# Kernel optimization log

Hardware: AMD Instinct MI355X
Metric: run time of the kernel (lower is better)

The kernel has to match this reference:

```python
import jax, jax.numpy as jnp
import numpy as np

VOCAB = 32000
D_MODEL = 1024


def setup_inputs() -> dict:
    key = jax.random.key(0)
    k = jax.random.split(key, 8)
    B, H, T, S = 8, 16, 128, 512
    src = jax.random.randint(k[0], (B, S), 0, VOCAB)
    decode_output = jax.random.normal(k[1], (B, T, D_MODEL), dtype=jnp.float32)
    decode_attn = jax.random.uniform(k[2], (B, H, T, S), dtype=jnp.float32)
    memory = jax.random.normal(k[3], (B, S, D_MODEL), dtype=jnp.float32)
    W_gen = jax.random.normal(k[4], (VOCAB, D_MODEL), dtype=jnp.float32) * (1.0 / np.sqrt(D_MODEL))
    b_gen = jnp.zeros((VOCAB,), dtype=jnp.float32)
    W_prob = jax.random.normal(k[5], (1, 2 * D_MODEL), dtype=jnp.float32) * (1.0 / np.sqrt(2 * D_MODEL))
    b_prob = jnp.zeros((1,), dtype=jnp.float32)
    return {"src": src, "decode_output": decode_output, "decode_attn": decode_attn,
            "memory": memory, "W_gen": W_gen, "b_gen": b_gen,
            "W_prob": W_prob, "b_prob": b_prob}


def reference(src, decode_output, decode_attn, memory, W_gen, b_gen, W_prob, b_prob):
    # mean over heads: [B, T, S]
    attn = jnp.mean(decode_attn, axis=1)
    B, T, S = attn.shape
    V = W_gen.shape[0]

    # generation logits: [B, T, V]
    gen_logits = jnp.einsum('btd,vd->btv', decode_output, W_gen) + b_gen

    # context vector: [B, T, D]
    context = jnp.einsum('bts,bsd->btd', attn, memory)

    # scatter-add copy distribution over vocab: [B, T, V]
    src_exp = jnp.broadcast_to(src[:, None, :], (B, T, S))  # token ids per step
    b_idx = jnp.arange(B)[:, None, None]
    t_idx = jnp.arange(T)[None, :, None]
    copy_logits = jnp.zeros((B, T, V), dtype=attn.dtype).at[b_idx, t_idx, src_exp].add(attn)

    # copy gate: sigmoid(Linear([context; decode_output])) -> [B, T, 1]
    cat = jnp.concatenate([context, decode_output], axis=-1)
    prob = jax.nn.sigmoid(jnp.einsum('btd,od->bto', cat, W_prob) + b_prob)

    gen_p = prob * jax.nn.softmax(gen_logits, axis=-1)
    copy_p = (1.0 - prob) * jax.nn.softmax(copy_logits, axis=-1)
    final = gen_p + copy_p
    return jnp.log(final).reshape(-1, V)
```

## Files before the change

### kernel.cpp

```cpp
#include <hip/hip_runtime.h>
#include <hip/hip_bf16.h>
#include <cstddef>
#include <cstdint>

#define BB 8
#define HH 16
#define TT 128
#define SS 512
#define DD 1024
#define VV 32000
#define MM (BB * TT)

typedef float f32x4 __attribute__((ext_vector_type(4)));
typedef short short8v __attribute__((ext_vector_type(8)));
typedef unsigned short ushort8v __attribute__((ext_vector_type(8)));

__device__ __forceinline__ unsigned short f2bf(float x) {
    __hip_bfloat16 h = __float2bfloat16(x);
    return __builtin_bit_cast(unsigned short, h);
}
__device__ __forceinline__ float bf2f(unsigned short u) {
    unsigned int x = ((unsigned int)u) << 16;
    return __builtin_bit_cast(float, x);
}

__device__ __forceinline__ float wave_sum(float v) {
#pragma unroll
    for (int o = 1; o < 64; o <<= 1) v += __shfl_xor(v, o);
    return v;
}
__device__ __forceinline__ float wave_max(float v) {
#pragma unroll
    for (int o = 1; o < 64; o <<= 1) v = fmaxf(v, __shfl_xor(v, o));
    return v;
}
__device__ __forceinline__ float block_sum(float v, float* red, int tid) {
    v = wave_sum(v);
    __syncthreads();
    if ((tid & 63) == 0) red[tid >> 6] = v;
    __syncthreads();
    return red[0] + red[1] + red[2] + red[3];
}
__device__ __forceinline__ float block_max(float v, float* red, int tid) {
    v = wave_max(v);
    __syncthreads();
    if ((tid & 63) == 0) red[tid >> 6] = v;
    __syncthreads();
    return fmaxf(fmaxf(red[0], red[1]), fmaxf(red[2], red[3]));
}

__global__ void k_pm_init(int* pos_map, float* zg) {
    int i = blockIdx.x * 256 + threadIdx.x;
    if (i < BB * VV) pos_map[i] = 0x7fffffff;
    if (i < MM) zg[i] = 0.0f;
}

__global__ void k_pm_build(const int* __restrict__ src, int* pos_map) {
    int b = blockIdx.x, s = threadIdx.x;
    int tok = src[b * SS + s];
    atomicMin(&pos_map[b * VV + tok], s);
}

__global__ __launch_bounds__(256) void k_cast(const float* __restrict__ in,
                                              unsigned short* __restrict__ outp, int n8) {
    int stride = gridDim.x * 256;
    for (int i = blockIdx.x * 256 + threadIdx.x; i < n8; i += stride) {
        const float4* p = reinterpret_cast<const float4*>(in + (size_t)i * 8);
        float4 a = p[0], b = p[1];
        ushort8v u;
        u[0] = f2bf(a.x); u[1] = f2bf(a.y); u[2] = f2bf(a.z); u[3] = f2bf(a.w);
        u[4] = f2bf(b.x); u[5] = f2bf(b.y); u[6] = f2bf(b.z); u[7] = f2bf(b.w);
        *reinterpret_cast<ushort8v*>(outp + (size_t)i * 8) = u;
    }
}

__global__ __launch_bounds__(256) void k_vecdots(const float* __restrict__ memory,
                                                 const float* __restrict__ dec,
                                                 const float* __restrict__ wprob,
                                                 float* mw, float* dw) {
    int row = blockIdx.x * 4 + (threadIdx.x >> 6);
    int lane = threadIdx.x & 63;
    const float4* srcv;
    const float4* wv;
    if (row < BB * SS) {
        srcv = reinterpret_cast<const float4*>(memory + (size_t)row * DD);
        wv = reinterpret_cast<const float4*>(wprob);
    } else {
        srcv = reinterpret_cast<const float4*>(dec + (size_t)(row - BB * SS) * DD);
        wv = reinterpret_cast<const float4*>(wprob + DD);
    }
    float sum = 0.f;
#pragma unroll
    for (int k = 0; k < 4; ++k) {
        int idx = lane + 64 * k;
        float4 a = srcv[idx];
        float4 w = wv[idx];
        sum += a.x * w.x + a.y * w.y + a.z * w.z + a.w * w.w;
    }
    sum = wave_sum(sum);
    if (lane == 0) {
        if (row < BB * SS) mw[row] = sum;
        else dw[row - BB * SS] = sum;
    }
}

__global__ __launch_bounds__(256) void k_row(const float* __restrict__ dattn,
                                             const int* __restrict__ src,
                                             const int* __restrict__ pos_map,
                                             const float* __restrict__ mw,
                                             const float* __restrict__ dw,
                                             const float* __restrict__ bprob,
                                             float* __restrict__ e_vals,
                                             float* __restrict__ prob,
                                             float* __restrict__ zc,
                                             float* __restrict__ c0) {
    int bt = blockIdx.x;
    int b = bt >> 7;
    int t = bt & 127;
    int tid = threadIdx.x;
    __shared__ float a_row[SS];
    __shared__ float vals[SS];
    __shared__ float red[4];

    for (int s = tid; s < SS; s += 256) {
        const float* base = dattn + ((size_t)b * HH * TT + t) * SS + s;
        float sum = 0.f;
#pragma unroll
        for (int h = 0; h < HH; ++h) sum += base[(size_t)h * TT * SS];
        a_row[s] = sum * 0.0625f;
        vals[s] = 0.f;
    }
    __syncthreads();
    for (int s = tid; s < SS; s += 256) {
        int rep = pos_map[b * VV + src[b * SS + s]];
        atomicAdd(&vals[rep], a_row[s]);
    }
    __syncthreads();
    float psum = 0.f;
    for (int s = tid; s < SS; s += 256) psum += a_row[s] * mw[b * SS + s];
    psum = block_sum(psum, red, tid);
    float z = psum + dw[bt] + bprob[0];
    float p = 1.0f / (1.0f + __expf(-z));
    float mxv = -3.4e38f;
    for (int s = tid; s < SS; s += 256) {
        int rep = pos_map[b * VV + src[b * SS + s]];
        if (rep == s) mxv = fmaxf(mxv, vals[s]);
    }
    mxv = block_max(mxv, red, tid);
    float m_c = fmaxf(0.0f, mxv);
    float sexp = 0.f, cnt = 0.f;
    for (int s = tid; s < SS; s += 256) {
        int rep = pos_map[b * VV + src[b * SS + s]];
        float e = 0.0f;
        if (rep == s) {
            e = __expf(vals[s] - m_c);
            sexp += e;
            cnt += 1.0f;
        }
        e_vals[(size_t)bt * SS + s] = e;
    }
    sexp = block_sum(sexp, red, tid);
    cnt = block_sum(cnt, red, tid);
    if (tid == 0) {
        prob[bt] = p;
        zc[bt] = ((float)VV - cnt) * __expf(-m_c) + sexp;
        c0[bt] = __expf(-m_c);
    }
}

#define NKT 32
#define BUFE 12288

#define AS1 __attribute__((address_space(1)))
#define AS3 __attribute__((address_space(3)))

template <int EPI>
__global__ __launch_bounds__(512, 4) void k_gemm_bf(const unsigned short* __restrict__ Abf,
                                                    const unsigned short* __restrict__ Wbf,
                                                    const float* __restrict__ bgen,
                                                    float* __restrict__ out,
                                                    unsigned short* __restrict__ ebuf,
                                                    float* __restrict__ zg) {
    __shared__ unsigned short lds[3 * BUFE];

    int tid = threadIdx.x;
    int p = blockIdx.x;
    int wgid = (p & 7) * 125 + (p >> 3);
    int mt = wgid & 7, nt = wgid >> 3;
    int m0 = mt * 128, v0 = nt * 256;

    int lane = tid & 63, w = tid >> 6;
    int wm = w & 1, wn = w >> 1;

    int srow = tid >> 2;
    int schunk = (tid & 3) ^ ((tid >> 3) & 3);
    const unsigned short* gA = Abf + (size_t)(m0 + srow) * DD + schunk * 8;
    const unsigned short* gB = Wbf + (size_t)(v0 + srow) * DD + schunk * 8;

#define STAGE(T, BI) do {                                                              \
    size_t ko_ = (size_t)(T) * 32;                                                     \
    __builtin_amdgcn_global_load_lds(                                                  \
        (const AS1 void*)(gA + ko_),                                                   \
        (AS3 void*)(lds + (BI) * BUFE + tid * 8), 16, 0, 0);                           \
    __builtin_amdgcn_global_load_lds(                                                  \
        (const AS1 void*)(gB + ko_),                                                   \
        (AS3 void*)(lds + (BI) * BUFE + 4096 + tid * 8), 16, 0, 0);                    \
    __builtin_amdgcn_global_load_lds(                                                  \
        (const AS1 void*)(gB + (size_t)128 * DD + ko_),                                \
        (AS3 void*)(lds + (BI) * BUFE + 8192 + tid * 8), 16, 0, 0);                    \
} while (0)

    int lr = lane & 15, kg = lane >> 4;
    int xr = (lr >> 1) & 3;
    const unsigned short* arow = lds + (wm * 64 + lr) * 32 + ((kg ^ xr) << 3);
    const unsigned short* brow = lds + 4096 + (wn * 64 + lr) * 32 + ((kg ^ xr) << 3);

    f32x4 acc[4][4] = {};

#define ITER(T, BI, DO_STAGE, VM)  do {                                                \
    __builtin_amdgcn_s_barrier();                                                      \
    short8v af[4], bfr[4];                                                             \
    _Pragma("unroll")                                                                  \
    for (int i = 0; i < 4; ++i)                                                        \
        af[i] = *reinterpret_cast<const short8v*>(arow + (BI) * BUFE + i * 512);       \
    _Pragma("unroll")                                                                  \
    for (int j = 0; j < 4; ++j)                                                        \
        bfr[j] = *reinterpret_cast<const short8v*>(brow + (BI) * BUFE + j * 512);      \
    if (DO_STAGE) STAGE((T) + 2, ((BI) + 2) % 3);                                      \
    asm volatile("s_waitcnt lgkmcnt(0)" ::: "memory");                                 \
    __builtin_amdgcn_sched_barrier(0);                                                 \
    __builtin_amdgcn_s_setprio(1);                                                     \
    _Pragma("unroll")                                                                  \
    for (int i = 0; i < 4; ++i)                                                        \
        _Pragma("unroll")                                                              \
        for (int j = 0; j < 4; ++j)                                                    \
            acc[i][j] = __builtin_amdgcn_mfma_f32_16x16x32_bf16(af[i], bfr[j], acc[i][j], 0, 0, 0); \
    __builtin_amdgcn_s_setprio(0);                                                     \
    if ((VM) == 3) asm volatile("s_waitcnt vmcnt(3)" ::: "memory");                    \
    else if ((VM) == 0) asm volatile("s_waitcnt vmcnt(0)" ::: "memory");               \
} while (0)

    STAGE(0, 0);
    STAGE(1, 1);
    asm volatile("s_waitcnt vmcnt(3)" ::: "memory");

    for (int t = 0; t < NKT - 2; t += 3) {
        ITER(t + 0, 0, true, 3);
        ITER(t + 1, 1, true, 3);
        ITER(t + 2, 2, true, 3);
    }
    ITER(30, 0, false, 0);
    ITER(31, 1, false, -1);
#undef ITER
#undef STAGE

    int colb = lane & 15, rgrp = lane >> 4;
#pragma unroll
    for (int i = 0; i < 4; ++i) {
        float es0 = 0.f, es1 = 0.f, es2 = 0.f, es3 = 0.f;
        int gmb = m0 + wm * 64 + i * 16 + rgrp * 4;
#pragma unroll
        for (int j = 0; j < 4; ++j) {
            int gv = v0 + wn * 64 + j * 16 + colb;
            float bgj = bgen[gv];
            float v0f = acc[i][j][0] + bgj;
            float v1f = acc[i][j][1] + bgj;
            float v2f = acc[i][j][2] + bgj;
            float v3f = acc[i][j][3] + bgj;
            float e0 = __expf(v0f), e1 = __expf(v1f), e2 = __expf(v2f), e3 = __expf(v3f);
            if constexpr (EPI == 1) {
                ebuf[(size_t)(gmb + 0) * VV + gv] = f2bf(e0);
                ebuf[(size_t)(gmb + 1) * VV + gv] = f2bf(e1);
                ebuf[(size_t)(gmb + 2) * VV + gv] = f2bf(e2);
                ebuf[(size_t)(gmb + 3) * VV + gv] = f2bf(e3);
            } else {
                out[(size_t)(gmb + 0) * VV + gv] = v0f;
                out[(size_t)(gmb + 1) * VV + gv] = v1f;
                out[(size_t)(gmb + 2) * VV + gv] = v2f;
                out[(size_t)(gmb + 3) * VV + gv] = v3f;
            }
            es0 += e0; es1 += e1; es2 += e2; es3 += e3;
        }
        float es[4] = {es0, es1, es2, es3};
#pragma unroll
        for (int rr = 0; rr < 4; ++rr) {
            float e = es[rr];
            e += __shfl_xor(e, 1); e += __shfl_xor(e, 2);
            e += __shfl_xor(e, 4); e += __shfl_xor(e, 8);
            if (colb == 0) atomicAdd(&zg[gmb + rr], e);
        }
    }
}

#define FBb 128
#define FLDK 40

__global__ __launch_bounds__(256) void k_gemm_f32(const float* __restrict__ A,
                                                  const float* __restrict__ Wg,
                                                  const float* __restrict__ bgen,
                                                  float* __restrict__ out,
                                                  float* __restrict__ zg) {
    __shared__ unsigned short As[FBb * FLDK];
    __shared__ unsigned short Bs[FBb * FLDK];
    int tid = threadIdx.x;
    int bid = blockIdx.x;
    int mt = bid & 7;
    int nt = bid >> 3;
    int m0 = mt * FBb, v0 = nt * FBb;
    int lane = tid & 63, wid = tid >> 6;
    int wr = (wid >> 1) * 64, wc = (wid & 1) * 64;
    int lr = lane & 15, lk = (lane >> 4) << 3;
    int r = tid >> 1, c0 = (tid & 1) << 4;

    f32x4 acc[4][4] = {};

    for (int k0 = 0; k0 < DD; k0 += 32) {
        {
            const float4* pa = reinterpret_cast<const float4*>(A + (size_t)(m0 + r) * DD + k0 + c0);
            float4 x0 = pa[0], x1 = pa[1], x2 = pa[2], x3 = pa[3];
            ushort8v u0, u1;
            u0[0] = f2bf(x0.x); u0[1] = f2bf(x0.y); u0[2] = f2bf(x0.z); u0[3] = f2bf(x0.w);
            u0[4] = f2bf(x1.x); u0[5] = f2bf(x1.y); u0[6] = f2bf(x1.z); u0[7] = f2bf(x1.w);
            u1[0] = f2bf(x2.x); u1[1] = f2bf(x2.y); u1[2] = f2bf(x2.z); u1[3] = f2bf(x2.w);
            u1[4] = f2bf(x3.x); u1[5] = f2bf(x3.y); u1[6] = f2bf(x3.z); u1[7] = f2bf(x3.w);
            *reinterpret_cast<ushort8v*>(&As[r * FLDK + c0]) = u0;
            *reinterpret_cast<ushort8v*>(&As[r * FLDK + c0 + 8]) = u1;

            const float4* pb = reinterpret_cast<const float4*>(Wg + (size_t)(v0 + r) * DD + k0 + c0);
            float4 y0 = pb[0], y1 = pb[1], y2 = pb[2], y3 = pb[3];
            ushort8v w0, w1;
            w0[0] = f2bf(y0.x); w0[1] = f2bf(y0.y); w0[2] = f2bf(y0.z); w0[3] = f2bf(y0.w);
            w0[4] = f2bf(y1.x); w0[5] = f2bf(y1.y); w0[6] = f2bf(y1.z); w0[7] = f2bf(y1.w);
            w1[0] = f2bf(y2.x); w1[1] = f2bf(y2.y); w1[2] = f2bf(y2.z); w1[3] = f2bf(y2.w);
            w1[4] = f2bf(y3.x); w1[5] = f2bf(y3.y); w1[6] = f2bf(y3.z); w1[7] = f2bf(y3.w);
            *reinterpret_cast<ushort8v*>(&Bs[r * FLDK + c0]) = w0;
            *reinterpret_cast<ushort8v*>(&Bs[r * FLDK + c0 + 8]) = w1;
        }
        __syncthreads();

        short8v af[4], bfr[4];
#pragma unroll
        for (int i = 0; i < 4; ++i)
            af[i] = *reinterpret_cast<const short8v*>(&As[(wr + i * 16 + lr) * FLDK + lk]);
#pragma unroll
        for (int j = 0; j < 4; ++j)
            bfr[j] = *reinterpret_cast<const short8v*>(&Bs[(wc + j * 16 + lr) * FLDK + lk]);
#pragma unroll
        for (int i = 0; i < 4; ++i)
#pragma unroll
            for (int j = 0; j < 4; ++j)
                acc[i][j] = __builtin_amdgcn_mfma_f32_16x16x32_bf16(af[i], bfr[j], acc[i][j], 0, 0, 0);
        __syncthreads();
    }

    int colb = lane & 15;
    int rgrp = lane >> 4;
#pragma unroll
    for (int i = 0; i < 4; ++i) {
        float es0 = 0.f, es1 = 0.f, es2 = 0.f, es3 = 0.f;
        int gmb = m0 + wr + i * 16 + rgrp * 4;
#pragma unroll
        for (int j = 0; j < 4; ++j) {
            int gv = v0 + wc + j * 16 + colb;
            float bgj = bgen[gv];
            float v0f = acc[i][j][0] + bgj;
            float v1f = acc[i][j][1] + bgj;
            float v2f = acc[i][j][2] + bgj;
            float v3f = acc[i][j][3] + bgj;
            out[(size_t)(gmb + 0) * VV + gv] = v0f;
            out[(size_t)(gmb + 1) * VV + gv] = v1f;
            out[(size_t)(gmb + 2) * VV + gv] = v2f;
            out[(size_t)(gmb + 3) * VV + gv] = v3f;
            es0 += __expf(v0f); es1 += __expf(v1f);
            es2 += __expf(v2f); es3 += __expf(v3f);
        }
        float es[4] = {es0, es1, es2, es3};
#pragma unroll
        for (int rr = 0; rr < 4; ++rr) {
            float e = es[rr];
            e += __shfl_xor(e, 1); e += __shfl_xor(e, 2);
            e += __shfl_xor(e, 4); e += __shfl_xor(e, 8);
            if (colb == 0) atomicAdd(&zg[gmb + rr], e);
        }
    }
}

template <int RD16>
__global__ __launch_bounds__(256) void k_final(float* __restrict__ gen,
                                               const unsigned short* __restrict__ ebuf,
                                               const int* __restrict__ pos_map,
                                               const float* __restrict__ e_vals,
                                               const float* __restrict__ prob,
                                               const float* __restrict__ zc,
                                               const float* __restrict__ c0,
                                               const float* __restrict__ zg) {
    int m = blockIdx.x;
    int b = m >> 7;
    int tid = threadIdx.x;
    float p = prob[m];
    float A1 = p / zg[m];
    float A2 = (1.0f - p) / zc[m];
    float cc = c0[m];
    const float* ev = e_vals + (size_t)m * SS;
    float4* row = reinterpret_cast<float4*>(gen + (size_t)m * VV);
    const int4* pm = reinterpret_cast<const int4*>(pos_map + b * VV);
    if constexpr (RD16 == 1) {
        const ushort8v* erow = reinterpret_cast<const ushort8v*>(ebuf + (size_t)m * VV);
        for (int i = tid; i < VV / 8; i += 256) {
            ushort8v ee = erow[i];
            int4 rp0 = pm[2 * i], rp1 = pm[2 * i + 1];
            float4 o0, o1;
            o0.x = __logf(A1 * bf2f(ee[0]) + A2 * ((rp0.x < SS) ? ev[rp0.x] : cc));
            o0.y = __logf(A1 * bf2f(ee[1]) + A2 * ((rp0.y < SS) ? ev[rp0.y] : cc));
            o0.z = __logf(A1 * bf2f(ee[2]) + A2 * ((rp0.z < SS) ? ev[rp0.z] : cc));
            o0.w = __logf(A1 * bf2f(ee[3]) + A2 * ((rp0.w < SS) ? ev[rp0.w] : cc));
            o1.x = __logf(A1 * bf2f(ee[4]) + A2 * ((rp1.x < SS) ? ev[rp1.x] : cc));
            o1.y = __logf(A1 * bf2f(ee[5]) + A2 * ((rp1.y < SS) ? ev[rp1.y] : cc));
            o1.z = __logf(A1 * bf2f(ee[6]) + A2 * ((rp1.z < SS) ? ev[rp1.z] : cc));
            o1.w = __logf(A1 * bf2f(ee[7]) + A2 * ((rp1.w < SS) ? ev[rp1.w] : cc));
            row[2 * i] = o0;
            row[2 * i + 1] = o1;
        }
    } else {
        for (int i = tid; i < VV / 4; i += 256) {
            float4 g = row[i];
            int4 rp = pm[i];
            float4 o;
            o.x = __logf(A1 * __expf(g.x) + A2 * ((rp.x < SS) ? ev[rp.x] : cc));
            o.y = __logf(A1 * __expf(g.y) + A2 * ((rp.y < SS) ? ev[rp.y] : cc));
            o.z = __logf(A1 * __expf(g.z) + A2 * ((rp.z < SS) ? ev[rp.z] : cc));
            o.w = __logf(A1 * __expf(g.w) + A2 * ((rp.w < SS) ? ev[rp.w] : cc));
            row[i] = o;
        }
    }
}

extern "C" void kernel_launch(void* const* d_in, const int* in_sizes, int n_in,
                              void* d_out, int out_size, void* d_ws, size_t ws_size,
                              hipStream_t stream) {
    const int* src = (const int*)d_in[0];
    const float* dec = (const float*)d_in[1];
    const float* dattn = (const float*)d_in[2];
    const float* mem = (const float*)d_in[3];
    const float* wgen = (const float*)d_in[4];
    const float* bgen = (const float*)d_in[5];
    const float* wprob = (const float*)d_in[6];
    const float* bprob = (const float*)d_in[7];
    float* out = (float*)d_out;
    char* ws = (char*)d_ws;

    int* pos_map = (int*)(ws + 0);
    float* e_vals = (float*)(ws + 1048576);
    float* mw   = (float*)(ws + 3145728);
    float* dw   = (float*)(ws + 3145728 + 16384);
    float* prob = (float*)(ws + 3145728 + 20480);
    float* zc   = (float*)(ws + 3145728 + 24576);
    float* c0   = (float*)(ws + 3145728 + 28672);
    float* zg   = (float*)(ws + 3145728 + 32768);
    unsigned short* Wbf = (unsigned short*)(ws + 3211264);
    unsigned short* Abf = (unsigned short*)(ws + 3211264 + 65536000);
    unsigned short* Ebf = (unsigned short*)(ws + 3211264 + 65536000 + 2097152);
    const size_t NEEDED  = 3211264ull + 65536000ull + 2097152ull;
    const size_t NEEDED2 = NEEDED + 65536000ull;

    k_pm_init<<<(BB * VV + 255) / 256, 256, 0, stream>>>(pos_map, zg);
    k_pm_build<<<BB, SS, 0, stream>>>(src, pos_map);
    k_vecdots<<<(BB * SS + MM) / 4, 256, 0, stream>>>(mem, dec, wprob, mw, dw);
    k_row<<<MM, 256, 0, stream>>>(dattn, src, pos_map, mw, dw, bprob, e_vals, prob, zc, c0);

    if (ws_size >= NEEDED) {
        k_cast<<<2048, 256, 0, stream>>>(wgen, Wbf, VV * DD / 8);
        k_cast<<<512, 256, 0, stream>>>(dec, Abf, MM * DD / 8);
        if (ws_size >= NEEDED2) {
            k_gemm_bf<1><<<(MM / 128) * (VV / 256), 512, 0, stream>>>(Abf, Wbf, bgen, out, Ebf, zg);
            k_final<1><<<MM, 256, 0, stream>>>(out, Ebf, pos_map, e_vals, prob, zc, c0, zg);
        } else {
            k_gemm_bf<0><<<(MM / 128) * (VV / 256), 512, 0, stream>>>(Abf, Wbf, bgen, out, Ebf, zg);
            k_final<0><<<MM, 256, 0, stream>>>(out, Ebf, pos_map, e_vals, prob, zc, c0, zg);
        }
    } else {
        k_gemm_f32<<<(MM / FBb) * (VV / FBb), 256, 0, stream>>>(dec, wgen, bgen, out, zg);
        k_final<0><<<MM, 256, 0, stream>>>(out, Ebf, pos_map, e_vals, prob, zc, c0, zg);
    }
}
```

Baseline: 224.0 us.

## Merge setup kernels into one launch, vectorize head-mean loads, relax MFMA wait

Fuses position-map build, gate vector dots, and both bf16 casts into a single block-partitioned setup kernel, replacing four small launches with one. The head-mean loop in the row kernel now reads float2 per thread. In the GEMM inner step, A/B fragment loads are interleaved and the explicit lgkmcnt wait and sched_barrier are dropped so the compiler can overlap LDS reads with MFMAs. Removing the explicit wait relies on the compiler inserting the right waits; the fused kernel also runs the W cast on fewer, larger blocks.

```diff
diff --git a/kernel.cpp b/kernel.cpp
--- a/kernel.cpp
+++ b/kernel.cpp
@@ -55,52 +55,67 @@
     if (i < MM) zg[i] = 0.0f;
 }
 
-__global__ void k_pm_build(const int* __restrict__ src, int* pos_map) {
-    int b = blockIdx.x, s = threadIdx.x;
-    int tok = src[b * SS + s];
-    atomicMin(&pos_map[b * VV + tok], s);
-}
-
-__global__ __launch_bounds__(256) void k_cast(const float* __restrict__ in,
-                                              unsigned short* __restrict__ outp, int n8) {
-    int stride = gridDim.x * 256;
-    for (int i = blockIdx.x * 256 + threadIdx.x; i < n8; i += stride) {
-        const float4* p = reinterpret_cast<const float4*>(in + (size_t)i * 8);
-        float4 a = p[0], b = p[1];
-        ushort8v u;
-        u[0] = f2bf(a.x); u[1] = f2bf(a.y); u[2] = f2bf(a.z); u[3] = f2bf(a.w);
-        u[4] = f2bf(b.x); u[5] = f2bf(b.y); u[6] = f2bf(b.z); u[7] = f2bf(b.w);
-        *reinterpret_cast<ushort8v*>(outp + (size_t)i * 8) = u;
-    }
-}
-
-__global__ __launch_bounds__(256) void k_vecdots(const float* __restrict__ memory,
-                                                 const float* __restrict__ dec,
-                                                 const float* __restrict__ wprob,
-                                                 float* mw, float* dw) {
-    int row = blockIdx.x * 4 + (threadIdx.x >> 6);
-    int lane = threadIdx.x & 63;
-    const float4* srcv;
-    const float4* wv;
-    if (row < BB * SS) {
-        srcv = reinterpret_cast<const float4*>(memory + (size_t)row * DD);
-        wv = reinterpret_cast<const float4*>(wprob);
+__global__ __launch_bounds__(512) void k_setup(const int* __restrict__ src,
+                                               int* __restrict__ pos_map,
+                                               const float* __restrict__ memory,
+                                               const float* __restrict__ dec,
+                                               const float* __restrict__ wprob,
+                                               float* __restrict__ mw,
+                                               float* __restrict__ dw,
+                                               const float* __restrict__ wgen,
+                                               unsigned short* __restrict__ Wbf,
+                                               unsigned short* __restrict__ Abf) {
+    int blk = blockIdx.x, tid = threadIdx.x;
+    if (blk < 8) {
+        int tok = src[blk * SS + tid];
+        atomicMin(&pos_map[blk * VV + tok], tid);
+    } else if (blk < 648) {
+        int row = (blk - 8) * 8 + (tid >> 6);
+        int lane = tid & 63;
+        const float4* srcv;
+        const float4* wv;
+        if (row < BB * SS) {
+            srcv = reinterpret_cast<const float4*>(memory + (size_t)row * DD);
+            wv = reinterpret_cast<const float4*>(wprob);
+        } else {
+            srcv = reinterpret_cast<const float4*>(dec + (size_t)(row - BB * SS) * DD);
+            wv = reinterpret_cast<const float4*>(wprob + DD);
+        }
+        float sum = 0.f;
+#pragma unroll
+        for (int k = 0; k < 4; ++k) {
+            int idx = lane + 64 * k;
+            float4 a = srcv[idx];
+            float4 w = wv[idx];
+            sum += a.x * w.x + a.y * w.y + a.z * w.z + a.w * w.w;
+        }
+        sum = wave_sum(sum);
+        if (lane == 0) {
+            if (row < BB * SS) mw[row] = sum;
+            else dw[row - BB * SS] = sum;
+        }
+    } else if (blk < 1160) {
+        if (Wbf == nullptr) return;
+        const int n8 = VV * DD / 8;
+        for (int i = (blk - 648) * 512 + tid; i < n8; i += 512 * 512) {
+            const float4* p = reinterpret_cast<const float4*>(wgen + (size_t)i * 8);
+            float4 a = p[0], b = p[1];
+            ushort8v u;
+            u[0] = f2bf(a.x); u[1] = f2bf(a.y); u[2] = f2bf(a.z); u[3] = f2bf(a.w);
+            u[4] = f2bf(b.x); u[5] = f2bf(b.y); u[6] = f2bf(b.z); u[7] = f2bf(b.w);
+            *reinterpret_cast<ushort8v*>(Wbf + (size_t)i * 8) = u;
+        }
     } else {
-        srcv = reinterpret_cast<const float4*>(dec + (size_t)(row - BB * SS) * DD);
-        wv = reinterpret_cast<const float4*>(wprob + DD);
-    }
-    float sum = 0.f;
-#pragma unroll
-    for (int k = 0; k < 4; ++k) {
-        int idx = lane + 64 * k;
-        float4 a = srcv[idx];
-        float4 w = wv[idx];
-        sum += a.x * w.x + a.y * w.y + a.z * w.z + a.w * w.w;
-    }
-    sum = wave_sum(sum);
-    if (lane == 0) {
-        if (row < BB * SS) mw[row] = sum;
-        else dw[row - BB * SS] = sum;
+        if (Abf == nullptr) return;
+        const int n8 = MM * DD / 8;
+        for (int i = (blk - 1160) * 512 + tid; i < n8; i += 32 * 512) {
+            const float4* p = reinterpret_cast<const float4*>(dec + (size_t)i * 8);
+            float4 a = p[0], b = p[1];
+            ushort8v u;
+            u[0] = f2bf(a.x); u[1] = f2bf(a.y); u[2] = f2bf(a.z); u[3] = f2bf(a.w);
+            u[4] = f2bf(b.x); u[5] = f2bf(b.y); u[6] = f2bf(b.z); u[7] = f2bf(b.w);
+            *reinterpret_cast<ushort8v*>(Abf + (size_t)i * 8) = u;
+        }
     }
 }
 
@@ -122,13 +137,19 @@
     __shared__ float vals[SS];
     __shared__ float red[4];
 
-    for (int s = tid; s < SS; s += 256) {
-        const float* base = dattn + ((size_t)b * HH * TT + t) * SS + s;
-        float sum = 0.f;
-#pragma unroll
-        for (int h = 0; h < HH; ++h) sum += base[(size_t)h * TT * SS];
-        a_row[s] = sum * 0.0625f;
-        vals[s] = 0.f;
+    {
+        const float2* base = reinterpret_cast<const float2*>(
+            dattn + ((size_t)b * HH * TT + t) * SS) + tid;
+        float sx = 0.f, sy = 0.f;
+#pragma unroll
+        for (int h = 0; h < HH; ++h) {
+            float2 v = base[(size_t)h * (TT * SS / 2)];
+            sx += v.x; sy += v.y;
+        }
+        a_row[2 * tid] = sx * 0.0625f;
+        a_row[2 * tid + 1] = sy * 0.0625f;
+        vals[2 * tid] = 0.f;
+        vals[2 * tid + 1] = 0.f;
     }
     __syncthreads();
     for (int s = tid; s < SS; s += 256) {
@@ -221,14 +242,11 @@
     __builtin_amdgcn_s_barrier();                                                      \
     short8v af[4], bfr[4];                                                             \
     _Pragma("unroll")                                                                  \
-    for (int i = 0; i < 4; ++i)                                                        \
+    for (int i = 0; i < 4; ++i) {                                                      \
         af[i] = *reinterpret_cast<const short8v*>(arow + (BI) * BUFE + i * 512);       \
-    _Pragma("unroll")                                                                  \
-    for (int j = 0; j < 4; ++j)                                                        \
-        bfr[j] = *reinterpret_cast<const short8v*>(brow + (BI) * BUFE + j * 512);      \
+        bfr[i] = *reinterpret_cast<const short8v*>(brow + (BI) * BUFE + i * 512);      \
+    }                                                                                  \
     if (DO_STAGE) STAGE((T) + 2, ((BI) + 2) % 3);                                      \
-    asm volatile("s_waitcnt lgkmcnt(0)" ::: "memory");                                 \
-    __builtin_amdgcn_sched_barrier(0);                                                 \
     __builtin_amdgcn_s_setprio(1);                                                     \
     _Pragma("unroll")                                                                  \
     for (int i = 0; i < 4; ++i)                                                        \
@@ -463,14 +481,15 @@
     const size_t NEEDED  = 3211264ull + 65536000ull + 2097152ull;
     const size_t NEEDED2 = NEEDED + 65536000ull;
 
+    bool do_cast = ws_size >= NEEDED;
+
     k_pm_init<<<(BB * VV + 255) / 256, 256, 0, stream>>>(pos_map, zg);
-    k_pm_build<<<BB, SS, 0, stream>>>(src, pos_map);
-    k_vecdots<<<(BB * SS + MM) / 4, 256, 0, stream>>>(mem, dec, wprob, mw, dw);
+    k_setup<<<do_cast ? 1192 : 648, 512, 0, stream>>>(
+        src, pos_map, mem, dec, wprob, mw, dw, wgen,
+        do_cast ? Wbf : nullptr, do_cast ? Abf : nullptr);
     k_row<<<MM, 256, 0, stream>>>(dattn, src, pos_map, mw, dw, bprob, e_vals, prob, zc, c0);
 
-    if (ws_size >= NEEDED) {
-        k_cast<<<2048, 256, 0, stream>>>(wgen, Wbf, VV * DD / 8);
-        k_cast<<<512, 256, 0, stream>>>(dec, Abf, MM * DD / 8);
+    if (do_cast) {
         if (ws_size >= NEEDED2) {
             k_gemm_bf<1><<<(MM / 128) * (VV / 256), 512, 0, stream>>>(Abf, Wbf, bgen, out, Ebf, zg);
             k_final<1><<<MM, 256, 0, stream>>>(out, Ebf, pos_map, e_vals, prob, zc, c0, zg);
```

Result: no change. 225.1 us (+0.5%).
